# Kernel tuning notes

Measured on AMD Instinct MI355X. Metric: run time of the kernel, lower is better.

Reference implementation:

```python
import jax, jax.numpy as jnp
import numpy as np

N_NODES = 20000
N_EDGES = 320000
NUM_RELS = 16
IN_FEAT = 256
OUT_FEAT = 256


def setup_inputs() -> dict:
    key = jax.random.key(0)
    k_h, k_w, k_n, k_s, k_d, k_r = jax.random.split(key, 6)
    h = jax.random.normal(k_h, (N_NODES, IN_FEAT), dtype=jnp.float32)
    weight = jax.random.normal(k_w, (NUM_RELS, IN_FEAT, OUT_FEAT), dtype=jnp.float32)
    norm = jax.random.uniform(k_n, (N_EDGES, 1), dtype=jnp.float32)
    src = jax.random.randint(k_s, (N_EDGES,), 0, N_NODES, dtype=jnp.int32)
    dst = jax.random.randint(k_d, (N_EDGES,), 0, N_NODES, dtype=jnp.int32)
    rel_type = jax.random.randint(k_r, (N_EDGES,), 0, NUM_RELS, dtype=jnp.int32)
    return {"h": h, "weight": weight, "norm": norm, "src": src, "dst": dst, "rel_type": rel_type}


def reference(h, weight, norm, src, dst, rel_type):
    # Transform every node feature by every relation weight once ([R, N, O]),
    # instead of gathering a full [E, in, out] weight tensor per edge.
    transformed = jnp.einsum('ni,rio->rno', h, weight)
    # Per-edge message: h[src] @ W[rel] scaled by edge norm -> [E, O]
    msg = transformed[rel_type, src] * norm
    # Scatter-sum messages into destination nodes (DGL mailbox sum reduce).
    out = jax.ops.segment_sum(msg, dst, num_segments=h.shape[0])
    # bias=None, activation=None in this configuration, so apply_func is identity.
    return out
```

## Files before the change

kernel.cpp:

```cpp
#include <hip/hip_runtime.h>
#include <stdint.h>

#define N_NODES_C 20000
#define N_EDGES_C 320000
#define NUM_RELS_C 16
#define FEAT_C 256
#define CAP_LOG2 6
#define WS_FAST_BYTES 186497152ULL

typedef __bf16 bf16_t;
typedef __bf16 bf16x8 __attribute__((ext_vector_type(8)));
typedef __bf16 bf16x4 __attribute__((ext_vector_type(4)));
typedef float f32x4 __attribute__((ext_vector_type(4)));

__device__ __forceinline__ void async_load16(const void* g, void* l) {
  __builtin_amdgcn_global_load_lds(
      (__attribute__((address_space(1))) void*)const_cast<void*>(g),
      (__attribute__((address_space(3))) void*)l, 16, 0, 0);
}

__global__ void prep_fast_kernel(const float* __restrict__ h, bf16_t* __restrict__ hB,
                                 const float* __restrict__ W, bf16_t* __restrict__ Wt,
                                 const int* __restrict__ dst, const int* __restrict__ src,
                                 const int* __restrict__ rel, const float* __restrict__ norm,
                                 int* __restrict__ cnt, int2* __restrict__ bkt) {
  int b = blockIdx.x;
  int t = threadIdx.x;
  if (b < 5000) {
    int i = (b * 256 + t) * 4;
    float4 v = *(const float4*)(h + i);
    bf16x4 o = { (bf16_t)v.x, (bf16_t)v.y, (bf16_t)v.z, (bf16_t)v.w };
    *(bf16x4*)(hB + i) = o;
  } else if (b < 5256) {
    __shared__ bf16_t lds[64][66];
    int b2 = b - 5000;
    int r  = b2 >> 4;
    int i0 = ((b2 >> 2) & 3) << 6;
    int o0 = (b2 & 3) << 6;
    int tx = t & 15;
    int ty = t >> 4;
#pragma unroll
    for (int pass = 0; pass < 4; ++pass) {
      int il = ty + pass * 16;
      float4 v = *(const float4*)(W + (r << 16) + ((i0 + il) << 8) + o0 + tx * 4);
      lds[tx * 4 + 0][il] = (bf16_t)v.x;
      lds[tx * 4 + 1][il] = (bf16_t)v.y;
      lds[tx * 4 + 2][il] = (bf16_t)v.z;
      lds[tx * 4 + 3][il] = (bf16_t)v.w;
    }
    __syncthreads();
#pragma unroll
    for (int pass = 0; pass < 4; ++pass) {
      int ol = ty + pass * 16;
      bf16x4 pk = { lds[ol][tx * 4 + 0], lds[ol][tx * 4 + 1],
                    lds[ol][tx * 4 + 2], lds[ol][tx * 4 + 3] };
      *(bf16x4*)(Wt + (r << 16) + ((o0 + ol) << 8) + i0 + tx * 4) = pk;
    }
  } else {
    int e = (b - 5256) * 256 + t;
    if (e < N_EDGES_C) {
      int d = dst[e];
      int pos = (d << CAP_LOG2) + atomicAdd(&cnt[d], 1);
      int2 pk;
      pk.x = src[e] | (rel[e] << 16);
      pk.y = __float_as_int(norm[e]);
      bkt[pos] = pk;
    }
  }
}

__global__ void prep_kernel(const float* __restrict__ h, bf16_t* __restrict__ hB,
                            const float* __restrict__ W, bf16_t* __restrict__ Wt,
                            const int* __restrict__ dst, int* __restrict__ dcur) {
  int b = blockIdx.x;
  int t = threadIdx.x;
  if (b < 5000) {
    int i = (b * 256 + t) * 4;
    float4 v = *(const float4*)(h + i);
    bf16x4 o = { (bf16_t)v.x, (bf16_t)v.y, (bf16_t)v.z, (bf16_t)v.w };
    *(bf16x4*)(hB + i) = o;
  } else if (b < 9096) {
    int g = (b - 5000) * 256 + t;
    int i = g & 255;
    int o = (g >> 8) & 255;
    int r = g >> 16;
    Wt[(r << 16) + (o << 8) + i] = (bf16_t)W[(r << 16) + (i << 8) + o];
  } else {
    int e = (b - 9096) * 256 + t;
    if (e < N_EDGES_C) atomicAdd(&dcur[dst[e]], 1);
  }
}

__global__ void scan_dst_kernel(int* __restrict__ dcur, int* __restrict__ dstart) {
  __shared__ unsigned short cnt[20224];
  __shared__ int wsum[4];
  const int CH = 79;
  int t = threadIdx.x;
  int base = t * CH;
  int sum = 0;
  for (int i = 0; i < CH; ++i) {
    int idx = base + i;
    int c = (idx < N_NODES_C) ? dcur[idx] : 0;
    cnt[idx] = (unsigned short)c;
    sum += c;
  }
  int v = sum;
#pragma unroll
  for (int off = 1; off < 64; off <<= 1) {
    int u = __shfl_up(v, off);
    if ((t & 63) >= off) v += u;
  }
  if ((t & 63) == 63) wsum[t >> 6] = v;
  __syncthreads();
  int add = 0;
  for (int w = 0; w < (t >> 6); ++w) add += wsum[w];
  int run = v - sum + add;
  for (int i = 0; i < CH; ++i) {
    int idx = base + i;
    if (idx < N_NODES_C) {
      int c = cnt[idx];
      dstart[idx] = run;
      dcur[idx] = run;
      run += c;
    }
  }
  if (t == 0) dstart[N_NODES_C] = N_EDGES_C;
}

__global__ void bucket_dst_kernel(const int* __restrict__ dst, const int* __restrict__ src,
                                  const int* __restrict__ rel, const float* __restrict__ norm,
                                  int* __restrict__ dcur, int2* __restrict__ bkt) {
  int e = blockIdx.x * blockDim.x + threadIdx.x;
  if (e < N_EDGES_C) {
    int pos = atomicAdd(&dcur[dst[e]], 1);
    int2 pk;
    pk.x = src[e] | (rel[e] << 16);
    pk.y = __float_as_int(norm[e]);
    bkt[pos] = pk;
  }
}

__global__ __launch_bounds__(256) void gemm_t_kernel(
    const bf16_t* __restrict__ hB, const bf16_t* __restrict__ Wt,
    bf16_t* __restrict__ Tb) {
  int bx = blockIdx.x;
  int sub = bx & 31;
  int m0 = (bx >> 5) << 7;
  int r  = sub >> 1;
  int n0 = (sub & 1) << 7;

  __shared__ bf16_t Asm[3 * 128 * 32];
  __shared__ bf16_t Bsm[3 * 128 * 32];

  int tid = threadIdx.x;
  int lrow = tid >> 2;
  int pch = tid & 3;
  int rA0 = lrow, rA1 = lrow + 64;
  int lc0 = pch ^ ((rA0 >> 1) & 3);
  int lc1 = pch ^ ((rA1 >> 1) & 3);
  int gr0 = m0 + rA0; if (gr0 > N_NODES_C - 1) gr0 = N_NODES_C - 1;
  int gr1 = m0 + rA1; if (gr1 > N_NODES_C - 1) gr1 = N_NODES_C - 1;
  const char* gA0 = (const char*)(hB + (size_t)gr0 * FEAT_C) + lc0 * 16;
  const char* gA1 = (const char*)(hB + (size_t)gr1 * FEAT_C) + lc1 * 16;
  const char* gB0 = (const char*)(Wt + ((size_t)r * 256 + n0 + rA0) * FEAT_C) + lc0 * 16;
  const char* gB1 = (const char*)(Wt + ((size_t)r * 256 + n0 + rA1) * FEAT_C) + lc1 * 16;

  int wave = tid >> 6;
  int lane = tid & 63;
  int lq = lane >> 4;
  int lr = lane & 15;
  int wm = (wave >> 1) * 64;
  int wn = (wave & 1) * 64;
  int pc8 = (lq ^ ((lr >> 1) & 3)) * 8;

  f32x4 acc[4][4] = {};

#define STAGE(buf, t)                                             \
  do {                                                            \
    int kb_ = (t) * 64;                                           \
    char* aB_ = (char*)Asm + (buf) * 8192 + wave * 1024;          \
    char* bB_ = (char*)Bsm + (buf) * 8192 + wave * 1024;          \
    async_load16(gA0 + kb_, aB_);                                 \
    async_load16(gA1 + kb_, aB_ + 4096);                          \
    async_load16(gB0 + kb_, bB_);                                 \
    async_load16(gB1 + kb_, bB_ + 4096);                          \
  } while (0)

  STAGE(0, 0);
  STAGE(1, 1);

#pragma unroll
  for (int kk = 0; kk < 8; ++kk) {
    if (kk < 7) asm volatile("s_waitcnt vmcnt(4)" ::: "memory");
    else        asm volatile("s_waitcnt vmcnt(0)" ::: "memory");
    __builtin_amdgcn_s_barrier();
    __builtin_amdgcn_sched_barrier(0);
    const bf16_t* Ac = Asm + (kk % 3) * 4096;
    const bf16_t* Bc = Bsm + (kk % 3) * 4096;
    bf16x8 af[4], bfr[4];
#pragma unroll
    for (int mt = 0; mt < 4; ++mt) {
      int row = wm + mt * 16 + lr;
      af[mt] = *(const bf16x8*)&Ac[row * 32 + pc8];
    }
#pragma unroll
    for (int nt2 = 0; nt2 < 4; ++nt2) {
      int row = wn + nt2 * 16 + lr;
      bfr[nt2] = *(const bf16x8*)&Bc[row * 32 + pc8];
    }
    if (kk < 6) STAGE((kk + 2) % 3, kk + 2);
#pragma unroll
    for (int mt = 0; mt < 4; ++mt)
#pragma unroll
      for (int nt2 = 0; nt2 < 4; ++nt2)
        acc[mt][nt2] = __builtin_amdgcn_mfma_f32_16x16x32_bf16(af[mt], bfr[nt2], acc[mt][nt2], 0, 0, 0);
  }
#undef STAGE

#pragma unroll
  for (int mt = 0; mt < 4; ++mt) {
#pragma unroll
    for (int a = 0; a < 2; ++a) {
      int rg0 = a * 2, rg1 = rg0 + 1;
      union { bf16x4 v; long long u; } q0, q1;
      q0.v = (bf16x4){ (bf16_t)acc[mt][0][rg0], (bf16_t)acc[mt][1][rg0],
                       (bf16_t)acc[mt][2][rg0], (bf16_t)acc[mt][3][rg0] };
      q1.v = (bf16x4){ (bf16_t)acc[mt][0][rg1], (bf16_t)acc[mt][1][rg1],
                       (bf16_t)acc[mt][2][rg1], (bf16_t)acc[mt][3][rg1] };
      int odd = lr & 1;
      long long send = odd ? q0.u : q1.u;
      long long got = __shfl_xor(send, 1);
      union { bf16x8 v; long long u[2]; } w;
      w.u[0] = odd ? got : q0.u;
      w.u[1] = odd ? q1.u : got;
      int rg = rg0 + odd;
      int row = m0 + wm + mt * 16 + lq * 4 + rg;
      if (row < N_NODES_C) {
        int pos = n0 + wn + ((lr >> 1) << 3);
        *(bf16x8*)(Tb + (((size_t)r * N_NODES_C + row) << 8) + pos) = w.v;
      }
    }
  }
}

template <int MODE>
__global__ __launch_bounds__(256) void aggregate_kernel(
    const bf16_t* __restrict__ Tb, const int* __restrict__ meta,
    const int2* __restrict__ bkt, float* __restrict__ out) {
  int tid = threadIdx.x;
  int d = blockIdx.x * 4 + (tid >> 6);
  int lane = tid & 63;
  int h = lane >> 5;
  int l5 = lane & 31;
  int p0, p1;
  if (MODE == 0) { p0 = meta[d]; p1 = meta[d + 1]; }
  else           { p0 = d << CAP_LOG2; p1 = p0 + meta[d]; }
  int boff = l5 << 4;
  float A0[8] = {}, A1[8] = {}, A2[8] = {}, A3[8] = {};
  int p = p0 + h;
  for (; p + 6 < p1; p += 8) {
    int2 e0 = bkt[p];
    int2 e1 = bkt[p + 2];
    int2 e2 = bkt[p + 4];
    int2 e3 = bkt[p + 6];
    bf16x8 v0 = *(const bf16x8*)((const char*)(Tb + (((size_t)(e0.x >> 16) * N_NODES_C + (e0.x & 0xFFFF)) << 8)) + boff);
    bf16x8 v1 = *(const bf16x8*)((const char*)(Tb + (((size_t)(e1.x >> 16) * N_NODES_C + (e1.x & 0xFFFF)) << 8)) + boff);
    bf16x8 v2 = *(const bf16x8*)((const char*)(Tb + (((size_t)(e2.x >> 16) * N_NODES_C + (e2.x & 0xFFFF)) << 8)) + boff);
    bf16x8 v3 = *(const bf16x8*)((const char*)(Tb + (((size_t)(e3.x >> 16) * N_NODES_C + (e3.x & 0xFFFF)) << 8)) + boff);
    float n0 = __int_as_float(e0.y), n1 = __int_as_float(e1.y);
    float n2 = __int_as_float(e2.y), n3 = __int_as_float(e3.y);
#pragma unroll
    for (int j = 0; j < 8; ++j) {
      A0[j] += (float)v0[j] * n0;
      A1[j] += (float)v1[j] * n1;
      A2[j] += (float)v2[j] * n2;
      A3[j] += (float)v3[j] * n3;
    }
  }
  for (; p < p1; p += 2) {
    int2 e0 = bkt[p];
    bf16x8 v0 = *(const bf16x8*)((const char*)(Tb + (((size_t)(e0.x >> 16) * N_NODES_C + (e0.x & 0xFFFF)) << 8)) + boff);
    float n0 = __int_as_float(e0.y);
#pragma unroll
    for (int j = 0; j < 8; ++j) A0[j] += (float)v0[j] * n0;
  }
  float s[8];
#pragma unroll
  for (int j = 0; j < 8; ++j) {
    s[j] = (A0[j] + A1[j]) + (A2[j] + A3[j]);
    s[j] += __shfl_xor(s[j], 32);
  }
  if (h == 0) {
    int g64 = (l5 >> 3) << 6;
    int lr4 = (l5 << 1) & 15;
    float* o = out + (size_t)d * FEAT_C + g64 + lr4;
#pragma unroll
    for (int j = 0; j < 4; ++j) {
      float2 w = { s[j], s[j + 4] };
      *(float2*)(o + j * 16) = w;
    }
  }
}

extern "C" void kernel_launch(void* const* d_in, const int* in_sizes, int n_in,
                              void* d_out, int out_size, void* d_ws, size_t ws_size,
                              hipStream_t stream) {
  const float* h    = (const float*)d_in[0];
  const float* W    = (const float*)d_in[1];
  const float* norm = (const float*)d_in[2];
  const int*   src  = (const int*)d_in[3];
  const int*   dst  = (const int*)d_in[4];
  const int*   rel  = (const int*)d_in[5];
  float* out = (float*)d_out;

  char* ws = (char*)d_ws;
  bf16_t* hB   = (bf16_t*)ws;
  bf16_t* Wt   = (bf16_t*)(ws + 10240000);
  bf16_t* Tb   = (bf16_t*)(ws + 12337152);

  if (ws_size >= WS_FAST_BYTES) {
    int* cnt  = (int*)(ws + 176177152);
    int2* bkt = (int2*)(ws + 176257152);
    hipMemsetAsync(cnt, 0, N_NODES_C * sizeof(int), stream);
    prep_fast_kernel<<<6506, 256, 0, stream>>>(h, hB, W, Wt, dst, src, rel, norm, cnt, bkt);
    gemm_t_kernel<<<dim3(157 * 32, 1, 1), 256, 0, stream>>>(hB, Wt, Tb);
    aggregate_kernel<1><<<5000, 256, 0, stream>>>(Tb, cnt, bkt, out);
  } else {
    int* dstart  = (int*)(ws + 176177152);
    int* dcur    = (int*)(ws + 176257168);
    int2* bkt    = (int2*)(ws + 176337168);
    hipMemsetAsync(dcur, 0, N_NODES_C * sizeof(int), stream);
    prep_kernel<<<10346, 256, 0, stream>>>(h, hB, W, Wt, dst, dcur);
    scan_dst_kernel<<<1, 256, 0, stream>>>(dcur, dstart);
    bucket_dst_kernel<<<1250, 256, 0, stream>>>(dst, src, rel, norm, dcur, bkt);
    gemm_t_kernel<<<dim3(157 * 32, 1, 1), 256, 0, stream>>>(hB, Wt, Tb);
    aggregate_kernel<0><<<5000, 256, 0, stream>>>(Tb, dstart, bkt, out);
  }
}
```

Measured before the change: 186.1 us.

## Move edge bucketing into GEMM launch, fold memset into prep, deepen aggregate loads

Edge bucketing moves out of the prep kernel and into extra blocks appended to the GEMM launch, so the atomic scatter can overlap with the tiled GEMM. The hipMemsetAsync of the count array is replaced by clearing it inside the prep kernel, which removes one launch. The aggregate loop now issues 8 gathered loads per iteration into a single accumulator instead of 4 loads into four accumulators. The trade-offs are longer floating-point dependency chains and higher register pressure in the aggregate kernel, and the bucket blocks compete with GEMM blocks for compute units.

```diff
diff --git a/kernel.cpp b/kernel.cpp
--- a/kernel.cpp
+++ b/kernel.cpp
@@ -6,6 +6,7 @@
 #define NUM_RELS_C 16
 #define FEAT_C 256
 #define CAP_LOG2 6
+#define GEMM_BLOCKS 5024
 #define WS_FAST_BYTES 186497152ULL
 
 typedef __bf16 bf16_t;
@@ -21,9 +22,7 @@
 
 __global__ void prep_fast_kernel(const float* __restrict__ h, bf16_t* __restrict__ hB,
                                  const float* __restrict__ W, bf16_t* __restrict__ Wt,
-                                 const int* __restrict__ dst, const int* __restrict__ src,
-                                 const int* __restrict__ rel, const float* __restrict__ norm,
-                                 int* __restrict__ cnt, int2* __restrict__ bkt) {
+                                 int* __restrict__ cnt) {
   int b = blockIdx.x;
   int t = threadIdx.x;
   if (b < 5000) {
@@ -57,15 +56,8 @@
       *(bf16x4*)(Wt + (r << 16) + ((o0 + ol) << 8) + i0 + tx * 4) = pk;
     }
   } else {
-    int e = (b - 5256) * 256 + t;
-    if (e < N_EDGES_C) {
-      int d = dst[e];
-      int pos = (d << CAP_LOG2) + atomicAdd(&cnt[d], 1);
-      int2 pk;
-      pk.x = src[e] | (rel[e] << 16);
-      pk.y = __float_as_int(norm[e]);
-      bkt[pos] = pk;
-    }
+    int idx = (b - 5256) * 256 + t;
+    if (idx < N_NODES_C) cnt[idx] = 0;
   }
 }
 
@@ -140,10 +132,28 @@
   }
 }
 
-__global__ __launch_bounds__(256) void gemm_t_kernel(
+__global__ __launch_bounds__(256) void gemm_bucket_kernel(
     const bf16_t* __restrict__ hB, const bf16_t* __restrict__ Wt,
-    bf16_t* __restrict__ Tb) {
+    bf16_t* __restrict__ Tb,
+    const int* __restrict__ dst, const int* __restrict__ src,
+    const int* __restrict__ rel, const float* __restrict__ norm,
+    int* __restrict__ cnt, int2* __restrict__ bkt) {
   int bx = blockIdx.x;
+  int tid = threadIdx.x;
+
+  if (bx >= GEMM_BLOCKS) {
+    int e = (bx - GEMM_BLOCKS) * 256 + tid;
+    if (e < N_EDGES_C) {
+      int d = dst[e];
+      int pos = (d << CAP_LOG2) + atomicAdd(&cnt[d], 1);
+      int2 pk;
+      pk.x = src[e] | (rel[e] << 16);
+      pk.y = __float_as_int(norm[e]);
+      bkt[pos] = pk;
+    }
+    return;
+  }
+
   int sub = bx & 31;
   int m0 = (bx >> 5) << 7;
   int r  = sub >> 1;
@@ -152,7 +162,6 @@
   __shared__ bf16_t Asm[3 * 128 * 32];
   __shared__ bf16_t Bsm[3 * 128 * 32];
 
-  int tid = threadIdx.x;
   int lrow = tid >> 2;
   int pch = tid & 3;
   int rA0 = lrow, rA1 = lrow + 64;
@@ -256,38 +265,44 @@
   if (MODE == 0) { p0 = meta[d]; p1 = meta[d + 1]; }
   else           { p0 = d << CAP_LOG2; p1 = p0 + meta[d]; }
   int boff = l5 << 4;
-  float A0[8] = {}, A1[8] = {}, A2[8] = {}, A3[8] = {};
+  float acc[8] = {};
   int p = p0 + h;
-  for (; p + 6 < p1; p += 8) {
-    int2 e0 = bkt[p];
-    int2 e1 = bkt[p + 2];
-    int2 e2 = bkt[p + 4];
-    int2 e3 = bkt[p + 6];
-    bf16x8 v0 = *(const bf16x8*)((const char*)(Tb + (((size_t)(e0.x >> 16) * N_NODES_C + (e0.x & 0xFFFF)) << 8)) + boff);
-    bf16x8 v1 = *(const bf16x8*)((const char*)(Tb + (((size_t)(e1.x >> 16) * N_NODES_C + (e1.x & 0xFFFF)) << 8)) + boff);
-    bf16x8 v2 = *(const bf16x8*)((const char*)(Tb + (((size_t)(e2.x >> 16) * N_NODES_C + (e2.x & 0xFFFF)) << 8)) + boff);
-    bf16x8 v3 = *(const bf16x8*)((const char*)(Tb + (((size_t)(e3.x >> 16) * N_NODES_C + (e3.x & 0xFFFF)) << 8)) + boff);
-    float n0 = __int_as_float(e0.y), n1 = __int_as_float(e1.y);
-    float n2 = __int_as_float(e2.y), n3 = __int_as_float(e3.y);
-#pragma unroll
-    for (int j = 0; j < 8; ++j) {
-      A0[j] += (float)v0[j] * n0;
-      A1[j] += (float)v1[j] * n1;
-      A2[j] += (float)v2[j] * n2;
-      A3[j] += (float)v3[j] * n3;
-    }
-  }
-  for (; p < p1; p += 2) {
-    int2 e0 = bkt[p];
-    bf16x8 v0 = *(const bf16x8*)((const char*)(Tb + (((size_t)(e0.x >> 16) * N_NODES_C + (e0.x & 0xFFFF)) << 8)) + boff);
-    float n0 = __int_as_float(e0.y);
-#pragma unroll
-    for (int j = 0; j < 8; ++j) A0[j] += (float)v0[j] * n0;
+  for (; p + 14 < p1; p += 16) {
+    int2 m[8];
+#pragma unroll
+    for (int q = 0; q < 8; ++q) m[q] = bkt[p + 2 * q];
+    bf16x8 v[8];
+#pragma unroll
+    for (int q = 0; q < 8; ++q)
+      v[q] = *(const bf16x8*)((const char*)(Tb + (((size_t)(m[q].x >> 16) * N_NODES_C + (m[q].x & 0xFFFF)) << 8)) + boff);
+#pragma unroll
+    for (int q = 0; q < 8; ++q) {
+      float nq = __int_as_float(m[q].y);
+#pragma unroll
+      for (int j = 0; j < 8; ++j) acc[j] += (float)v[q][j] * nq;
+    }
+  }
+  for (; p + 2 < p1; p += 4) {
+    int2 m0 = bkt[p];
+    int2 m1 = bkt[p + 2];
+    bf16x8 v0 = *(const bf16x8*)((const char*)(Tb + (((size_t)(m0.x >> 16) * N_NODES_C + (m0.x & 0xFFFF)) << 8)) + boff);
+    bf16x8 v1 = *(const bf16x8*)((const char*)(Tb + (((size_t)(m1.x >> 16) * N_NODES_C + (m1.x & 0xFFFF)) << 8)) + boff);
+    float n0 = __int_as_float(m0.y);
+    float n1 = __int_as_float(m1.y);
+#pragma unroll
+    for (int j = 0; j < 8; ++j) acc[j] += (float)v0[j] * n0 + (float)v1[j] * n1;
+  }
+  if (p < p1) {
+    int2 m0 = bkt[p];
+    bf16x8 v0 = *(const bf16x8*)((const char*)(Tb + (((size_t)(m0.x >> 16) * N_NODES_C + (m0.x & 0xFFFF)) << 8)) + boff);
+    float n0 = __int_as_float(m0.y);
+#pragma unroll
+    for (int j = 0; j < 8; ++j) acc[j] += (float)v0[j] * n0;
   }
   float s[8];
 #pragma unroll
   for (int j = 0; j < 8; ++j) {
-    s[j] = (A0[j] + A1[j]) + (A2[j] + A3[j]);
+    s[j] = acc[j];
     s[j] += __shfl_xor(s[j], 32);
   }
   if (h == 0) {
@@ -321,9 +336,9 @@
   if (ws_size >= WS_FAST_BYTES) {
     int* cnt  = (int*)(ws + 176177152);
     int2* bkt = (int2*)(ws + 176257152);
-    hipMemsetAsync(cnt, 0, N_NODES_C * sizeof(int), stream);
-    prep_fast_kernel<<<6506, 256, 0, stream>>>(h, hB, W, Wt, dst, src, rel, norm, cnt, bkt);
-    gemm_t_kernel<<<dim3(157 * 32, 1, 1), 256, 0, stream>>>(hB, Wt, Tb);
+    prep_fast_kernel<<<5335, 256, 0, stream>>>(h, hB, W, Wt, cnt);
+    gemm_bucket_kernel<<<GEMM_BLOCKS + 1250, 256, 0, stream>>>(
+        hB, Wt, Tb, dst, src, rel, norm, cnt, bkt);
     aggregate_kernel<1><<<5000, 256, 0, stream>>>(Tb, cnt, bkt, out);
   } else {
     int* dstart  = (int*)(ws + 176177152);
@@ -333,7 +348,8 @@
     prep_kernel<<<10346, 256, 0, stream>>>(h, hB, W, Wt, dst, dcur);
     scan_dst_kernel<<<1, 256, 0, stream>>>(dcur, dstart);
     bucket_dst_kernel<<<1250, 256, 0, stream>>>(dst, src, rel, norm, dcur, bkt);
-    gemm_t_kernel<<<dim3(157 * 32, 1, 1), 256, 0, stream>>>(hB, Wt, Tb);
+    gemm_bucket_kernel<<<GEMM_BLOCKS, 256, 0, stream>>>(
+        hB, Wt, Tb, nullptr, nullptr, nullptr, nullptr, nullptr, nullptr);
     aggregate_kernel<0><<<5000, 256, 0, stream>>>(Tb, dstart, bkt, out);
   }
 }
```

Measured after the change: 184.8 us. No clear change (-0.7%).
